# Performance work log

Measured on AMD Instinct MI355X. Metric: run time of the kernel, lower is better.

Reference implementation:

```python
import jax, jax.numpy as jnp
import numpy as np

B, H, L, D = 8, 16, 1024, 64

def setup_inputs() -> dict:
    key = jax.random.key(0)
    kq, kk, kv = jax.random.split(key, 3)
    q = jax.random.normal(kq, (B, H, L, D), dtype=jnp.float32)
    k = jax.random.normal(kk, (B, H, L, D), dtype=jnp.float32)
    v = jax.random.normal(kv, (B, H, L, D), dtype=jnp.float32)
    # causal mask, broadcast over batch and head
    mask = jnp.tril(jnp.ones((L, L), dtype=jnp.int32))[None, None, :, :]
    return {"q": q, "k": k, "v": v, "mask": mask}

def reference(q, k, v, mask):
    b, h, l, d = q.shape
    # FAITHFUL to original: k.view(b, h, d, l) is a reshape, NOT a transpose
    k_t = k.reshape(b, h, d, l)
    score = jnp.matmul(q, k_t) / np.sqrt(d).astype(np.float32)  # [b,h,l,l]
    # FAITHFUL to original bug: masked_fill(mask==0, -e) with e=1e-12
    score = jnp.where(mask == 0, jnp.float32(-1e-12), score)
    attn = jax.nn.softmax(score, axis=-1)
    out = jnp.matmul(attn, v)  # [b,h,l,d]
    return (out, attn)
```

## Files before the change

kernel.cpp:

```cpp
#include <hip/hip_runtime.h>

#define L_  1024
#define D_  64
#define TM  128
#define TN  64
#define LDK 72
#define NT  (L_ / TN)

typedef __attribute__((ext_vector_type(8))) short          short8;
typedef __attribute__((ext_vector_type(8))) unsigned short ushort8;
typedef __attribute__((ext_vector_type(4))) float          f32x4;

__device__ __forceinline__ unsigned short bf16r(float f) {
    unsigned u = __builtin_bit_cast(unsigned, f);
    u += 0x7fffu + ((u >> 16) & 1u);
    return (unsigned short)(u >> 16);
}

__device__ __forceinline__ void barrier_lds() {
    asm volatile("s_waitcnt lgkmcnt(0)" ::: "memory");
    __builtin_amdgcn_s_barrier();
}

__global__ __launch_bounds__(256, 2)
void sdpa_kernel(const float* __restrict__ q, const float* __restrict__ kmat,
                 const float* __restrict__ v, float* __restrict__ out,
                 float* __restrict__ attn)
{
    __shared__ __align__(16) unsigned short Qs[TM * LDK];
    __shared__ __align__(16) unsigned short Ks[2][TN * LDK];
    __shared__ __align__(16) unsigned short Vs[2][D_ * LDK];
    __shared__ __align__(16) unsigned short Ps[TM * LDK];

    const int t    = threadIdx.x;
    const int wave = t >> 6;
    const int lane = t & 63;
    const int quad = lane >> 4;
    const int l15  = lane & 15;
    const int bh   = blockIdx.x;
    const int rty  = blockIdx.y;

    const float* qb = q    + (size_t)bh * (L_ * D_);
    const float* kb = kmat + (size_t)bh * (L_ * D_);
    const float* vb = v    + (size_t)bh * (L_ * D_);
    float* outb  = out  + (size_t)bh * (L_ * D_);
    float* attnb = attn + (size_t)bh * ((size_t)L_ * L_);

    const int ng = t & 31, kg = t >> 5;
    float2 rK[8], rV[8];

    auto loadK = [&](int nt) {
        const float* src = kb + (size_t)(kg * 8) * L_ + nt * TN + 2 * ng;
        #pragma unroll
        for (int j = 0; j < 8; ++j) rK[j] = *(const float2*)(src + (size_t)j * L_);
    };
    auto writeK = [&](unsigned short* dst) {
        ushort8 r0, r1;
        #pragma unroll
        for (int j = 0; j < 8; ++j) { r0[j] = bf16r(rK[j].x); r1[j] = bf16r(rK[j].y); }
        *(ushort8*)&dst[(2 * ng)     * LDK + kg * 8] = r0;
        *(ushort8*)&dst[(2 * ng + 1) * LDK + kg * 8] = r1;
    };
    auto loadV = [&](int nt) {
        const float* src = vb + (size_t)(nt * TN + kg * 8) * D_ + 2 * ng;
        #pragma unroll
        for (int j = 0; j < 8; ++j) rV[j] = *(const float2*)(src + (size_t)j * D_);
    };
    auto writeV = [&](unsigned short* dst) {
        ushort8 r0, r1;
        #pragma unroll
        for (int j = 0; j < 8; ++j) { r0[j] = bf16r(rV[j].x); r1[j] = bf16r(rV[j].y); }
        *(ushort8*)&dst[(2 * ng)     * LDK + kg * 8] = r0;
        *(ushort8*)&dst[(2 * ng + 1) * LDK + kg * 8] = r1;
    };

    const int rowA = wave * 32;

    auto computeScoreT = [&](f32x4 (&acc)[2][4], const unsigned short* ksrc) {
        #pragma unroll
        for (int ks = 0; ks < 2; ++ks) {
            const int cu = ks * 32 + quad * 8;
            short8 af[2];
            #pragma unroll
            for (int tr = 0; tr < 2; ++tr)
                af[tr] = *(const short8*)&Qs[(rowA + tr * 16 + l15) * LDK + cu];
            #pragma unroll
            for (int tc = 0; tc < 4; ++tc) {
                short8 bfr = *(const short8*)&ksrc[(tc * 16 + l15) * LDK + cu];
                #pragma unroll
                for (int tr = 0; tr < 2; ++tr)
                    acc[tr][tc] = __builtin_amdgcn_mfma_f32_16x16x32_bf16(bfr, af[tr], acc[tr][tc], 0, 0, 0);
            }
        }
    };

    const f32x4 zero4 = {0.f, 0.f, 0.f, 0.f};

    for (int pass = 0; pass < 2; ++pass) {
        const int rt = (pass == 0) ? rty : (7 - rty);
        const int m0 = rt * TM;

        barrier_lds();

        #pragma unroll
        for (int i = 0; i < 8; ++i) {
            int idx = (i * 256 + t) * 4;
            int m = idx >> 6, c = idx & 63;
            float4 f = *(const float4*)&qb[(size_t)(m0 + m) * D_ + c];
            ushort4 b;
            b.x = bf16r(f.x); b.y = bf16r(f.y); b.z = bf16r(f.z); b.w = bf16r(f.w);
            *(ushort4*)&Qs[m * LDK + c] = b;
        }

        float zpart[2][4] = {};
        const int ntmax1 = (m0 + TM - 1) / TN;
        loadK(0); writeK(Ks[0]);
        for (int nt = 0; nt <= ntmax1; ++nt) {
            barrier_lds();
            if (nt < ntmax1) loadK(nt + 1);
            f32x4 acc[2][4];
            #pragma unroll
            for (int tr = 0; tr < 2; ++tr)
                #pragma unroll
                for (int tc = 0; tc < 4; ++tc) acc[tr][tc] = zero4;
            computeScoreT(acc, Ks[nt & 1]);
            #pragma unroll
            for (int tr = 0; tr < 2; ++tr) {
                const int gm = m0 + rowA + tr * 16 + l15;
                #pragma unroll
                for (int tc = 0; tc < 4; ++tc)
                    #pragma unroll
                    for (int r = 0; r < 4; ++r) {
                        const int gn = nt * TN + tc * 16 + quad * 4 + r;
                        zpart[tr][tc] += (gn > gm) ? 1.0f : __expf(acc[tr][tc][r] * 0.125f);
                    }
            }
            if (nt < ntmax1) writeK(Ks[(nt + 1) & 1]);
        }
        const float zmissing = (float)(L_ - (ntmax1 + 1) * TN);

        loadK(0); loadV(0);
        float rcpz[2];
        #pragma unroll
        for (int tr = 0; tr < 2; ++tr) {
            float z = (zpart[tr][0] + zpart[tr][1]) + (zpart[tr][2] + zpart[tr][3]);
            z += __shfl_xor(z, 16);
            z += __shfl_xor(z, 32);
            rcpz[tr] = 1.0f / (z + zmissing);
        }
        barrier_lds();
        writeK(Ks[0]); writeV(Vs[0]);

        f32x4 oacc[2][4];
        #pragma unroll
        for (int tr = 0; tr < 2; ++tr)
            #pragma unroll
            for (int tc = 0; tc < 4; ++tc) oacc[tr][tc] = zero4;

        for (int nt = 0; nt < NT; ++nt) {
            const bool fullmask = (nt * TN) > (m0 + TM - 1);
            barrier_lds();
            const int nn = nt + 1;
            const bool nextV = (nn < NT);
            const bool nextK = nextV && ((nn * TN) <= (m0 + TM - 1));
            if (nextV) loadV(nn);
            if (nextK) loadK(nn);

            if (!fullmask) {
                f32x4 acc[2][4];
                #pragma unroll
                for (int tr = 0; tr < 2; ++tr)
                    #pragma unroll
                    for (int tc = 0; tc < 4; ++tc) acc[tr][tc] = zero4;
                computeScoreT(acc, Ks[nt & 1]);
                #pragma unroll
                for (int tr = 0; tr < 2; ++tr) {
                    const int lrow = rowA + tr * 16 + l15;
                    const int gm = m0 + lrow;
                    const float rz = rcpz[tr];
                    #pragma unroll
                    for (int tc = 0; tc < 4; ++tc) {
                        float p[4];
                        #pragma unroll
                        for (int r = 0; r < 4; ++r) {
                            const int gn = nt * TN + tc * 16 + quad * 4 + r;
                            float e = (gn > gm) ? 1.0f : __expf(acc[tr][tc][r] * 0.125f);
                            p[r] = e * rz;
                        }
                        float4 vv = {p[0], p[1], p[2], p[3]};
                        *(float4*)&attnb[(size_t)gm * L_ + nt * TN + tc * 16 + quad * 4] = vv;
                        ushort4 pw;
                        pw.x = bf16r(p[0]); pw.y = bf16r(p[1]);
                        pw.z = bf16r(p[2]); pw.w = bf16r(p[3]);
                        *(ushort4*)&Ps[lrow * LDK + tc * 16 + quad * 4] = pw;
                    }
                }
            } else {
                const bool firstFull = (nt == ntmax1 + 1);
                #pragma unroll
                for (int tr = 0; tr < 2; ++tr) {
                    const int lrow = rowA + tr * 16 + l15;
                    const int gm = m0 + lrow;
                    const float rz = rcpz[tr];
                    float4 vv = {rz, rz, rz, rz};
                    const unsigned short pb = bf16r(rz);
                    ushort4 p4; p4.x = pb; p4.y = pb; p4.z = pb; p4.w = pb;
                    #pragma unroll
                    for (int c = 0; c < 4; ++c) {
                        *(float4*)&attnb[(size_t)gm * L_ + nt * TN + c * 16 + quad * 4] = vv;
                        if (firstFull)
                            *(ushort4*)&Ps[lrow * LDK + c * 16 + quad * 4] = p4;
                    }
                }
            }

            #pragma unroll
            for (int ks = 0; ks < 2; ++ks) {
                const int cu = ks * 32 + quad * 8;
                short8 pf[2];
                #pragma unroll
                for (int tr = 0; tr < 2; ++tr)
                    pf[tr] = *(const short8*)&Ps[(rowA + tr * 16 + l15) * LDK + cu];
                #pragma unroll
                for (int tc = 0; tc < 4; ++tc) {
                    short8 vf = *(const short8*)&Vs[nt & 1][(tc * 16 + l15) * LDK + cu];
                    #pragma unroll
                    for (int tr = 0; tr < 2; ++tr)
                        oacc[tr][tc] = __builtin_amdgcn_mfma_f32_16x16x32_bf16(pf[tr], vf, oacc[tr][tc], 0, 0, 0);
                }
            }

            if (nextV) writeV(Vs[nn & 1]);
            if (nextK) writeK(Ks[nn & 1]);
        }

        #pragma unroll
        for (int tr = 0; tr < 2; ++tr)
            #pragma unroll
            for (int r = 0; r < 4; ++r) {
                const int gm = m0 + rowA + tr * 16 + quad * 4 + r;
                #pragma unroll
                for (int tc = 0; tc < 4; ++tc)
                    outb[(size_t)gm * D_ + tc * 16 + l15] = oacc[tr][tc][r];
            }
    }
}

extern "C" void kernel_launch(void* const* d_in, const int* in_sizes, int n_in,
                              void* d_out, int out_size, void* d_ws, size_t ws_size,
                              hipStream_t stream) {
    (void)in_sizes; (void)n_in; (void)d_ws; (void)ws_size; (void)out_size;
    const float* q = (const float*)d_in[0];
    const float* k = (const float*)d_in[1];
    const float* v = (const float*)d_in[2];
    float* out  = (float*)d_out;
    float* attn = (float*)d_out + (size_t)8 * 16 * 1024 * 64;
    dim3 grid(128, 4);
    sdpa_kernel<<<grid, dim3(256), 0, stream>>>(q, k, v, out, attn);
}
```

Measured before the change: 698.3 us.

## Fuse both row-tile passes into one loop sharing K/V tiles, keep Q in registers

Each block handles two query row tiles (rty and 7-rty). It now processes both in a single sweep over K/V tiles instead of two sequential passes, so every staged K/V tile is loaded, converted and barrier-synchronised once and used for both row tiles. The Q fragments move out of LDS into registers, preloaded once per block, which frees the Qs buffer and removes the per-pass Q staging. In exchange register pressure roughly doubles for the output accumulators and Q fragments under the 2-blocks-per-CU launch bound, which risks spills. Ps is also rewritten on every fully masked tile, because it is now shared between the two row tiles.

```diff
diff --git a/kernel.cpp b/kernel.cpp
--- a/kernel.cpp
+++ b/kernel.cpp
@@ -27,7 +27,6 @@
                  const float* __restrict__ v, float* __restrict__ out,
                  float* __restrict__ attn)
 {
-    __shared__ __align__(16) unsigned short Qs[TM * LDK];
     __shared__ __align__(16) unsigned short Ks[2][TN * LDK];
     __shared__ __align__(16) unsigned short Vs[2][D_ * LDK];
     __shared__ __align__(16) unsigned short Ps[TM * LDK];
@@ -39,6 +38,10 @@
     const int l15  = lane & 15;
     const int bh   = blockIdx.x;
     const int rty  = blockIdx.y;
+    const int m0A  = rty * TM;
+    const int m0B  = (7 - rty) * TM;
+    const int ntmaxA = 2 * rty + 1;
+    const int ntmaxB = 15 - 2 * rty;
 
     const float* qb = q    + (size_t)bh * (L_ * D_);
     const float* kb = kmat + (size_t)bh * (L_ * D_);
@@ -46,6 +49,30 @@
     float* outb  = out  + (size_t)bh * (L_ * D_);
     float* attnb = attn + (size_t)bh * ((size_t)L_ * L_);
 
+    const int rowA = wave * 32;
+
+    short8 qA[2][2], qB[2][2];
+    {
+        auto ldq = [&](int m0, short8 (&qr)[2][2]) {
+            #pragma unroll
+            for (int tr = 0; tr < 2; ++tr)
+                #pragma unroll
+                for (int ks = 0; ks < 2; ++ks) {
+                    const float* src = qb + (size_t)(m0 + rowA + tr * 16 + l15) * D_ + ks * 32 + quad * 8;
+                    float4 a = *(const float4*)src;
+                    float4 b = *(const float4*)(src + 4);
+                    short8 r;
+                    r[0] = (short)bf16r(a.x); r[1] = (short)bf16r(a.y);
+                    r[2] = (short)bf16r(a.z); r[3] = (short)bf16r(a.w);
+                    r[4] = (short)bf16r(b.x); r[5] = (short)bf16r(b.y);
+                    r[6] = (short)bf16r(b.z); r[7] = (short)bf16r(b.w);
+                    qr[tr][ks] = r;
+                }
+        };
+        ldq(m0A, qA);
+        ldq(m0B, qB);
+    }
+
     const int ng = t & 31, kg = t >> 5;
     float2 rK[8], rV[8];
 
@@ -74,176 +101,177 @@
         *(ushort8*)&dst[(2 * ng + 1) * LDK + kg * 8] = r1;
     };
 
-    const int rowA = wave * 32;
-
-    auto computeScoreT = [&](f32x4 (&acc)[2][4], const unsigned short* ksrc) {
+    auto computeScoreT = [&](f32x4 (&acc)[2][4], const short8 (&qr)[2][2],
+                             const unsigned short* ksrc) {
         #pragma unroll
         for (int ks = 0; ks < 2; ++ks) {
             const int cu = ks * 32 + quad * 8;
-            short8 af[2];
-            #pragma unroll
-            for (int tr = 0; tr < 2; ++tr)
-                af[tr] = *(const short8*)&Qs[(rowA + tr * 16 + l15) * LDK + cu];
             #pragma unroll
             for (int tc = 0; tc < 4; ++tc) {
                 short8 bfr = *(const short8*)&ksrc[(tc * 16 + l15) * LDK + cu];
                 #pragma unroll
                 for (int tr = 0; tr < 2; ++tr)
-                    acc[tr][tc] = __builtin_amdgcn_mfma_f32_16x16x32_bf16(bfr, af[tr], acc[tr][tc], 0, 0, 0);
+                    acc[tr][tc] = __builtin_amdgcn_mfma_f32_16x16x32_bf16(bfr, qr[tr][ks], acc[tr][tc], 0, 0, 0);
             }
         }
     };
 
     const f32x4 zero4 = {0.f, 0.f, 0.f, 0.f};
 
-    for (int pass = 0; pass < 2; ++pass) {
-        const int rt = (pass == 0) ? rty : (7 - rty);
-        const int m0 = rt * TM;
-
+    float zpA[2][4] = {}, zpB[2][4] = {};
+    auto accumZ = [&](f32x4 (&acc)[2][4], float (&zp)[2][4], int m0, int nt) {
+        #pragma unroll
+        for (int tr = 0; tr < 2; ++tr) {
+            const int gm = m0 + rowA + tr * 16 + l15;
+            #pragma unroll
+            for (int tc = 0; tc < 4; ++tc)
+                #pragma unroll
+                for (int r = 0; r < 4; ++r) {
+                    const int gn = nt * TN + tc * 16 + quad * 4 + r;
+                    zp[tr][tc] += (gn > gm) ? 1.0f : __expf(acc[tr][tc][r] * 0.125f);
+                }
+        }
+    };
+
+    loadK(0); writeK(Ks[0]);
+    for (int nt = 0; nt <= ntmaxB; ++nt) {
         barrier_lds();
-
-        #pragma unroll
-        for (int i = 0; i < 8; ++i) {
-            int idx = (i * 256 + t) * 4;
-            int m = idx >> 6, c = idx & 63;
-            float4 f = *(const float4*)&qb[(size_t)(m0 + m) * D_ + c];
-            ushort4 b;
-            b.x = bf16r(f.x); b.y = bf16r(f.y); b.z = bf16r(f.z); b.w = bf16r(f.w);
-            *(ushort4*)&Qs[m * LDK + c] = b;
-        }
-
-        float zpart[2][4] = {};
-        const int ntmax1 = (m0 + TM - 1) / TN;
-        loadK(0); writeK(Ks[0]);
-        for (int nt = 0; nt <= ntmax1; ++nt) {
-            barrier_lds();
-            if (nt < ntmax1) loadK(nt + 1);
+        if (nt < ntmaxB) loadK(nt + 1);
+        if (nt <= ntmaxA) {
             f32x4 acc[2][4];
             #pragma unroll
             for (int tr = 0; tr < 2; ++tr)
                 #pragma unroll
                 for (int tc = 0; tc < 4; ++tc) acc[tr][tc] = zero4;
-            computeScoreT(acc, Ks[nt & 1]);
+            computeScoreT(acc, qA, Ks[nt & 1]);
+            accumZ(acc, zpA, m0A, nt);
+        }
+        {
+            f32x4 acc[2][4];
+            #pragma unroll
+            for (int tr = 0; tr < 2; ++tr)
+                #pragma unroll
+                for (int tc = 0; tc < 4; ++tc) acc[tr][tc] = zero4;
+            computeScoreT(acc, qB, Ks[nt & 1]);
+            accumZ(acc, zpB, m0B, nt);
+        }
+        if (nt < ntmaxB) writeK(Ks[(nt + 1) & 1]);
+    }
+    const float zmissA = (float)(L_ - (ntmaxA + 1) * TN);
+    const float zmissB = (float)(L_ - (ntmaxB + 1) * TN);
+
+    loadK(0); loadV(0);
+    float rcpzA[2], rcpzB[2];
+    #pragma unroll
+    for (int tr = 0; tr < 2; ++tr) {
+        float za = (zpA[tr][0] + zpA[tr][1]) + (zpA[tr][2] + zpA[tr][3]);
+        za += __shfl_xor(za, 16);
+        za += __shfl_xor(za, 32);
+        rcpzA[tr] = 1.0f / (za + zmissA);
+        float zb = (zpB[tr][0] + zpB[tr][1]) + (zpB[tr][2] + zpB[tr][3]);
+        zb += __shfl_xor(zb, 16);
+        zb += __shfl_xor(zb, 32);
+        rcpzB[tr] = 1.0f / (zb + zmissB);
+    }
+    barrier_lds();
+    writeK(Ks[0]); writeV(Vs[0]);
+
+    f32x4 oA[2][4], oB[2][4];
+    #pragma unroll
+    for (int tr = 0; tr < 2; ++tr)
+        #pragma unroll
+        for (int tc = 0; tc < 4; ++tc) { oA[tr][tc] = zero4; oB[tr][tc] = zero4; }
+
+    auto doTile = [&](int nt, int m0, int ntmaxv, const short8 (&qr)[2][2],
+                      const float (&rz)[2], f32x4 (&oacc)[2][4]) {
+        if (nt <= ntmaxv) {
+            f32x4 acc[2][4];
+            #pragma unroll
+            for (int tr = 0; tr < 2; ++tr)
+                #pragma unroll
+                for (int tc = 0; tc < 4; ++tc) acc[tr][tc] = zero4;
+            computeScoreT(acc, qr, Ks[nt & 1]);
             #pragma unroll
             for (int tr = 0; tr < 2; ++tr) {
-                const int gm = m0 + rowA + tr * 16 + l15;
-                #pragma unroll
-                for (int tc = 0; tc < 4; ++tc)
+                const int lrow = rowA + tr * 16 + l15;
+                const int gm = m0 + lrow;
+                const float rzv = rz[tr];
+                #pragma unroll
+                for (int tc = 0; tc < 4; ++tc) {
+                    float p[4];
                     #pragma unroll
                     for (int r = 0; r < 4; ++r) {
                         const int gn = nt * TN + tc * 16 + quad * 4 + r;
-                        zpart[tr][tc] += (gn > gm) ? 1.0f : __expf(acc[tr][tc][r] * 0.125f);
+                        float e = (gn > gm) ? 1.0f : __expf(acc[tr][tc][r] * 0.125f);
+                        p[r] = e * rzv;
                     }
-            }
-            if (nt < ntmax1) writeK(Ks[(nt + 1) & 1]);
-        }
-        const float zmissing = (float)(L_ - (ntmax1 + 1) * TN);
-
-        loadK(0); loadV(0);
-        float rcpz[2];
-        #pragma unroll
-        for (int tr = 0; tr < 2; ++tr) {
-            float z = (zpart[tr][0] + zpart[tr][1]) + (zpart[tr][2] + zpart[tr][3]);
-            z += __shfl_xor(z, 16);
-            z += __shfl_xor(z, 32);
-            rcpz[tr] = 1.0f / (z + zmissing);
-        }
+                    float4 vv = {p[0], p[1], p[2], p[3]};
+                    *(float4*)&attnb[(size_t)gm * L_ + nt * TN + tc * 16 + quad * 4] = vv;
+                    ushort4 pw;
+                    pw.x = bf16r(p[0]); pw.y = bf16r(p[1]);
+                    pw.z = bf16r(p[2]); pw.w = bf16r(p[3]);
+                    *(ushort4*)&Ps[lrow * LDK + tc * 16 + quad * 4] = pw;
+                }
+            }
+        } else {
+            #pragma unroll
+            for (int tr = 0; tr < 2; ++tr) {
+                const int lrow = rowA + tr * 16 + l15;
+                const int gm = m0 + lrow;
+                const float rzv = rz[tr];
+                float4 vv = {rzv, rzv, rzv, rzv};
+                const unsigned short pb = bf16r(rzv);
+                ushort4 p4; p4.x = pb; p4.y = pb; p4.z = pb; p4.w = pb;
+                #pragma unroll
+                for (int c = 0; c < 4; ++c) {
+                    *(float4*)&attnb[(size_t)gm * L_ + nt * TN + c * 16 + quad * 4] = vv;
+                    *(ushort4*)&Ps[lrow * LDK + c * 16 + quad * 4] = p4;
+                }
+            }
+        }
+        #pragma unroll
+        for (int ks = 0; ks < 2; ++ks) {
+            const int cu = ks * 32 + quad * 8;
+            short8 pf[2];
+            #pragma unroll
+            for (int tr = 0; tr < 2; ++tr)
+                pf[tr] = *(const short8*)&Ps[(rowA + tr * 16 + l15) * LDK + cu];
+            #pragma unroll
+            for (int tc = 0; tc < 4; ++tc) {
+                short8 vf = *(const short8*)&Vs[nt & 1][(tc * 16 + l15) * LDK + cu];
+                #pragma unroll
+                for (int tr = 0; tr < 2; ++tr)
+                    oacc[tr][tc] = __builtin_amdgcn_mfma_f32_16x16x32_bf16(pf[tr], vf, oacc[tr][tc], 0, 0, 0);
+            }
+        }
+    };
+
+    for (int nt = 0; nt < NT; ++nt) {
         barrier_lds();
-        writeK(Ks[0]); writeV(Vs[0]);
-
-        f32x4 oacc[2][4];
-        #pragma unroll
-        for (int tr = 0; tr < 2; ++tr)
-            #pragma unroll
-            for (int tc = 0; tc < 4; ++tc) oacc[tr][tc] = zero4;
-
-        for (int nt = 0; nt < NT; ++nt) {
-            const bool fullmask = (nt * TN) > (m0 + TM - 1);
-            barrier_lds();
-            const int nn = nt + 1;
-            const bool nextV = (nn < NT);
-            const bool nextK = nextV && ((nn * TN) <= (m0 + TM - 1));
-            if (nextV) loadV(nn);
-            if (nextK) loadK(nn);
-
-            if (!fullmask) {
-                f32x4 acc[2][4];
-                #pragma unroll
-                for (int tr = 0; tr < 2; ++tr)
-                    #pragma unroll
-                    for (int tc = 0; tc < 4; ++tc) acc[tr][tc] = zero4;
-                computeScoreT(acc, Ks[nt & 1]);
-                #pragma unroll
-                for (int tr = 0; tr < 2; ++tr) {
-                    const int lrow = rowA + tr * 16 + l15;
-                    const int gm = m0 + lrow;
-                    const float rz = rcpz[tr];
-                    #pragma unroll
-                    for (int tc = 0; tc < 4; ++tc) {
-                        float p[4];
-                        #pragma unroll
-                        for (int r = 0; r < 4; ++r) {
-                            const int gn = nt * TN + tc * 16 + quad * 4 + r;
-                            float e = (gn > gm) ? 1.0f : __expf(acc[tr][tc][r] * 0.125f);
-                            p[r] = e * rz;
-                        }
-                        float4 vv = {p[0], p[1], p[2], p[3]};
-                        *(float4*)&attnb[(size_t)gm * L_ + nt * TN + tc * 16 + quad * 4] = vv;
-                        ushort4 pw;
-                        pw.x = bf16r(p[0]); pw.y = bf16r(p[1]);
-                        pw.z = bf16r(p[2]); pw.w = bf16r(p[3]);
-                        *(ushort4*)&Ps[lrow * LDK + tc * 16 + quad * 4] = pw;
-                    }
-                }
-            } else {
-                const bool firstFull = (nt == ntmax1 + 1);
-                #pragma unroll
-                for (int tr = 0; tr < 2; ++tr) {
-                    const int lrow = rowA + tr * 16 + l15;
-                    const int gm = m0 + lrow;
-                    const float rz = rcpz[tr];
-                    float4 vv = {rz, rz, rz, rz};
-                    const unsigned short pb = bf16r(rz);
-                    ushort4 p4; p4.x = pb; p4.y = pb; p4.z = pb; p4.w = pb;
-                    #pragma unroll
-                    for (int c = 0; c < 4; ++c) {
-                        *(float4*)&attnb[(size_t)gm * L_ + nt * TN + c * 16 + quad * 4] = vv;
-                        if (firstFull)
-                            *(ushort4*)&Ps[lrow * LDK + c * 16 + quad * 4] = p4;
-                    }
-                }
-            }
-
-            #pragma unroll
-            for (int ks = 0; ks < 2; ++ks) {
-                const int cu = ks * 32 + quad * 8;
-                short8 pf[2];
-                #pragma unroll
-                for (int tr = 0; tr < 2; ++tr)
-                    pf[tr] = *(const short8*)&Ps[(rowA + tr * 16 + l15) * LDK + cu];
-                #pragma unroll
-                for (int tc = 0; tc < 4; ++tc) {
-                    short8 vf = *(const short8*)&Vs[nt & 1][(tc * 16 + l15) * LDK + cu];
-                    #pragma unroll
-                    for (int tr = 0; tr < 2; ++tr)
-                        oacc[tr][tc] = __builtin_amdgcn_mfma_f32_16x16x32_bf16(pf[tr], vf, oacc[tr][tc], 0, 0, 0);
-                }
-            }
-
-            if (nextV) writeV(Vs[nn & 1]);
-            if (nextK) writeK(Ks[nn & 1]);
-        }
-
-        #pragma unroll
-        for (int tr = 0; tr < 2; ++tr)
-            #pragma unroll
-            for (int r = 0; r < 4; ++r) {
-                const int gm = m0 + rowA + tr * 16 + quad * 4 + r;
-                #pragma unroll
-                for (int tc = 0; tc < 4; ++tc)
-                    outb[(size_t)gm * D_ + tc * 16 + l15] = oacc[tr][tc][r];
-            }
-    }
+        const int nn = nt + 1;
+        const bool nextV = (nn < NT);
+        const bool nextK = nextV && (nn <= ntmaxB);
+        if (nextV) loadV(nn);
+        if (nextK) loadK(nn);
+
+        doTile(nt, m0A, ntmaxA, qA, rcpzA, oA);
+        doTile(nt, m0B, ntmaxB, qB, rcpzB, oB);
+
+        if (nextV) writeV(Vs[nn & 1]);
+        if (nextK) writeK(Ks[nn & 1]);
+    }
+
+    #pragma unroll
+    for (int tr = 0; tr < 2; ++tr)
+        #pragma unroll
+        for (int r = 0; r < 4; ++r) {
+            const int lr = rowA + tr * 16 + quad * 4 + r;
+            #pragma unroll
+            for (int tc = 0; tc < 4; ++tc) {
+                outb[(size_t)(m0A + lr) * D_ + tc * 16 + l15] = oA[tr][tc][r];
+                outb[(size_t)(m0B + lr) * D_ + tc * 16 + l15] = oB[tr][tc][r];
+            }
+        }
 }
 
 extern "C" void kernel_launch(void* const* d_in, const int* in_sizes, int n_in,
```

After: 742.8 us. +6.4%, slower.

## Use 8 waves per block with 16 rows each instead of 4 waves with 32

Applied to the files above, without the earlier changes.

Doubles the block to 512 threads so each wave handles one 16-row MFMA strip instead of two, halving per-thread accumulators and K/V staging registers. Global-to-LDS loads are spread over more threads. The aim is more waves in flight to hide memory latency on the attn write and K/V loads, at the cost of each wave reusing its K/V fragments across fewer rows and more LDS reads per MFMA.

```diff
diff --git a/kernel.cpp b/kernel.cpp
--- a/kernel.cpp
+++ b/kernel.cpp
@@ -8,7 +8,7 @@
 #define NT  (L_ / TN)
 
 typedef __attribute__((ext_vector_type(8))) short          short8;
-typedef __attribute__((ext_vector_type(8))) unsigned short ushort8;
+typedef __attribute__((ext_vector_type(4))) unsigned short ushort4e;
 typedef __attribute__((ext_vector_type(4))) float          f32x4;
 
 __device__ __forceinline__ unsigned short bf16r(float f) {
@@ -22,7 +22,7 @@
     __builtin_amdgcn_s_barrier();
 }
 
-__global__ __launch_bounds__(256, 2)
+__global__ __launch_bounds__(512, 4)
 void sdpa_kernel(const float* __restrict__ q, const float* __restrict__ kmat,
                  const float* __restrict__ v, float* __restrict__ out,
                  float* __restrict__ attn)
@@ -37,6 +37,7 @@
     const int lane = t & 63;
     const int quad = lane >> 4;
     const int l15  = lane & 15;
+    const int wrow = wave * 16;
     const int bh   = blockIdx.x;
     const int rty  = blockIdx.y;
 
@@ -47,49 +48,42 @@
     float* attnb = attn + (size_t)bh * ((size_t)L_ * L_);
 
     const int ng = t & 31, kg = t >> 5;
-    float2 rK[8], rV[8];
+    float2 rK[4], rV[4];
 
     auto loadK = [&](int nt) {
-        const float* src = kb + (size_t)(kg * 8) * L_ + nt * TN + 2 * ng;
-        #pragma unroll
-        for (int j = 0; j < 8; ++j) rK[j] = *(const float2*)(src + (size_t)j * L_);
+        const float* src = kb + (size_t)(kg * 4) * L_ + nt * TN + 2 * ng;
+        #pragma unroll
+        for (int j = 0; j < 4; ++j) rK[j] = *(const float2*)(src + (size_t)j * L_);
     };
     auto writeK = [&](unsigned short* dst) {
-        ushort8 r0, r1;
-        #pragma unroll
-        for (int j = 0; j < 8; ++j) { r0[j] = bf16r(rK[j].x); r1[j] = bf16r(rK[j].y); }
-        *(ushort8*)&dst[(2 * ng)     * LDK + kg * 8] = r0;
-        *(ushort8*)&dst[(2 * ng + 1) * LDK + kg * 8] = r1;
+        ushort4e r0, r1;
+        #pragma unroll
+        for (int j = 0; j < 4; ++j) { r0[j] = bf16r(rK[j].x); r1[j] = bf16r(rK[j].y); }
+        *(ushort4e*)&dst[(2 * ng)     * LDK + kg * 4] = r0;
+        *(ushort4e*)&dst[(2 * ng + 1) * LDK + kg * 4] = r1;
     };
     auto loadV = [&](int nt) {
-        const float* src = vb + (size_t)(nt * TN + kg * 8) * D_ + 2 * ng;
-        #pragma unroll
-        for (int j = 0; j < 8; ++j) rV[j] = *(const float2*)(src + (size_t)j * D_);
+        const float* src = vb + (size_t)(nt * TN + kg * 4) * D_ + 2 * ng;
+        #pragma unroll
+        for (int j = 0; j < 4; ++j) rV[j] = *(const float2*)(src + (size_t)j * D_);
     };
     auto writeV = [&](unsigned short* dst) {
-        ushort8 r0, r1;
-        #pragma unroll
-        for (int j = 0; j < 8; ++j) { r0[j] = bf16r(rV[j].x); r1[j] = bf16r(rV[j].y); }
-        *(ushort8*)&dst[(2 * ng)     * LDK + kg * 8] = r0;
-        *(ushort8*)&dst[(2 * ng + 1) * LDK + kg * 8] = r1;
-    };
-
-    const int rowA = wave * 32;
-
-    auto computeScoreT = [&](f32x4 (&acc)[2][4], const unsigned short* ksrc) {
+        ushort4e r0, r1;
+        #pragma unroll
+        for (int j = 0; j < 4; ++j) { r0[j] = bf16r(rV[j].x); r1[j] = bf16r(rV[j].y); }
+        *(ushort4e*)&dst[(2 * ng)     * LDK + kg * 4] = r0;
+        *(ushort4e*)&dst[(2 * ng + 1) * LDK + kg * 4] = r1;
+    };
+
+    auto computeScoreT = [&](f32x4 (&acc)[4], const unsigned short* ksrc) {
         #pragma unroll
         for (int ks = 0; ks < 2; ++ks) {
             const int cu = ks * 32 + quad * 8;
-            short8 af[2];
-            #pragma unroll
-            for (int tr = 0; tr < 2; ++tr)
-                af[tr] = *(const short8*)&Qs[(rowA + tr * 16 + l15) * LDK + cu];
+            short8 af = *(const short8*)&Qs[(wrow + l15) * LDK + cu];
             #pragma unroll
             for (int tc = 0; tc < 4; ++tc) {
                 short8 bfr = *(const short8*)&ksrc[(tc * 16 + l15) * LDK + cu];
-                #pragma unroll
-                for (int tr = 0; tr < 2; ++tr)
-                    acc[tr][tc] = __builtin_amdgcn_mfma_f32_16x16x32_bf16(bfr, af[tr], acc[tr][tc], 0, 0, 0);
+                acc[tc] = __builtin_amdgcn_mfma_f32_16x16x32_bf16(bfr, af, acc[tc], 0, 0, 0);
             }
         }
     };
@@ -103,59 +97,51 @@
         barrier_lds();
 
         #pragma unroll
-        for (int i = 0; i < 8; ++i) {
-            int idx = (i * 256 + t) * 4;
+        for (int i = 0; i < 4; ++i) {
+            int idx = (i * 512 + t) * 4;
             int m = idx >> 6, c = idx & 63;
             float4 f = *(const float4*)&qb[(size_t)(m0 + m) * D_ + c];
-            ushort4 b;
-            b.x = bf16r(f.x); b.y = bf16r(f.y); b.z = bf16r(f.z); b.w = bf16r(f.w);
-            *(ushort4*)&Qs[m * LDK + c] = b;
-        }
-
-        float zpart[2][4] = {};
+            ushort4e b;
+            b[0] = bf16r(f.x); b[1] = bf16r(f.y); b[2] = bf16r(f.z); b[3] = bf16r(f.w);
+            *(ushort4e*)&Qs[m * LDK + c] = b;
+        }
+
+        float zpart[4] = {};
         const int ntmax1 = (m0 + TM - 1) / TN;
         loadK(0); writeK(Ks[0]);
         for (int nt = 0; nt <= ntmax1; ++nt) {
             barrier_lds();
             if (nt < ntmax1) loadK(nt + 1);
-            f32x4 acc[2][4];
-            #pragma unroll
-            for (int tr = 0; tr < 2; ++tr)
-                #pragma unroll
-                for (int tc = 0; tc < 4; ++tc) acc[tr][tc] = zero4;
+            f32x4 acc[4];
+            #pragma unroll
+            for (int tc = 0; tc < 4; ++tc) acc[tc] = zero4;
             computeScoreT(acc, Ks[nt & 1]);
-            #pragma unroll
-            for (int tr = 0; tr < 2; ++tr) {
-                const int gm = m0 + rowA + tr * 16 + l15;
-                #pragma unroll
-                for (int tc = 0; tc < 4; ++tc)
-                    #pragma unroll
-                    for (int r = 0; r < 4; ++r) {
-                        const int gn = nt * TN + tc * 16 + quad * 4 + r;
-                        zpart[tr][tc] += (gn > gm) ? 1.0f : __expf(acc[tr][tc][r] * 0.125f);
-                    }
-            }
+            const int gm = m0 + wrow + l15;
+            #pragma unroll
+            for (int tc = 0; tc < 4; ++tc)
+                #pragma unroll
+                for (int r = 0; r < 4; ++r) {
+                    const int gn = nt * TN + tc * 16 + quad * 4 + r;
+                    zpart[tc] += (gn > gm) ? 1.0f : __expf(acc[tc][r] * 0.125f);
+                }
             if (nt < ntmax1) writeK(Ks[(nt + 1) & 1]);
         }
         const float zmissing = (float)(L_ - (ntmax1 + 1) * TN);
 
         loadK(0); loadV(0);
-        float rcpz[2];
-        #pragma unroll
-        for (int tr = 0; tr < 2; ++tr) {
-            float z = (zpart[tr][0] + zpart[tr][1]) + (zpart[tr][2] + zpart[tr][3]);
+        float rcpz;
+        {
+            float z = (zpart[0] + zpart[1]) + (zpart[2] + zpart[3]);
             z += __shfl_xor(z, 16);
             z += __shfl_xor(z, 32);
-            rcpz[tr] = 1.0f / (z + zmissing);
+            rcpz = 1.0f / (z + zmissing);
         }
         barrier_lds();
         writeK(Ks[0]); writeV(Vs[0]);
 
-        f32x4 oacc[2][4];
-        #pragma unroll
-        for (int tr = 0; tr < 2; ++tr)
-            #pragma unroll
-            for (int tc = 0; tc < 4; ++tc) oacc[tr][tc] = zero4;
+        f32x4 oacc[4];
+        #pragma unroll
+        for (int tc = 0; tc < 4; ++tc) oacc[tc] = zero4;
 
         for (int nt = 0; nt < NT; ++nt) {
             const bool fullmask = (nt * TN) > (m0 + TM - 1);
@@ -167,66 +153,51 @@
             if (nextK) loadK(nn);
 
             if (!fullmask) {
-                f32x4 acc[2][4];
-                #pragma unroll
-                for (int tr = 0; tr < 2; ++tr)
+                f32x4 acc[4];
+                #pragma unroll
+                for (int tc = 0; tc < 4; ++tc) acc[tc] = zero4;
+                computeScoreT(acc, Ks[nt & 1]);
+                const int lrow = wrow + l15;
+                const int gm = m0 + lrow;
+                #pragma unroll
+                for (int tc = 0; tc < 4; ++tc) {
+                    float p[4];
                     #pragma unroll
-                    for (int tc = 0; tc < 4; ++tc) acc[tr][tc] = zero4;
-                computeScoreT(acc, Ks[nt & 1]);
-                #pragma unroll
-                for (int tr = 0; tr < 2; ++tr) {
-                    const int lrow = rowA + tr * 16 + l15;
-                    const int gm = m0 + lrow;
-                    const float rz = rcpz[tr];
-                    #pragma unroll
-                    for (int tc = 0; tc < 4; ++tc) {
-                        float p[4];
-                        #pragma unroll
-                        for (int r = 0; r < 4; ++r) {
-                            const int gn = nt * TN + tc * 16 + quad * 4 + r;
-                            float e = (gn > gm) ? 1.0f : __expf(acc[tr][tc][r] * 0.125f);
-                            p[r] = e * rz;
-                        }
-                        float4 vv = {p[0], p[1], p[2], p[3]};
-                        *(float4*)&attnb[(size_t)gm * L_ + nt * TN + tc * 16 + quad * 4] = vv;
-                        ushort4 pw;
-                        pw.x = bf16r(p[0]); pw.y = bf16r(p[1]);
-                        pw.z = bf16r(p[2]); pw.w = bf16r(p[3]);
-                        *(ushort4*)&Ps[lrow * LDK + tc * 16 + quad * 4] = pw;
+                    for (int r = 0; r < 4; ++r) {
+                        const int gn = nt * TN + tc * 16 + quad * 4 + r;
+                        float e = (gn > gm) ? 1.0f : __expf(acc[tc][r] * 0.125f);
+                        p[r] = e * rcpz;
                     }
+                    float4 vv = {p[0], p[1], p[2], p[3]};
+                    *(float4*)&attnb[(size_t)gm * L_ + nt * TN + tc * 16 + quad * 4] = vv;
+                    ushort4e pw;
+                    pw[0] = bf16r(p[0]); pw[1] = bf16r(p[1]);
+                    pw[2] = bf16r(p[2]); pw[3] = bf16r(p[3]);
+                    *(ushort4e*)&Ps[lrow * LDK + tc * 16 + quad * 4] = pw;
                 }
             } else {
                 const bool firstFull = (nt == ntmax1 + 1);
-                #pragma unroll
-                for (int tr = 0; tr < 2; ++tr) {
-                    const int lrow = rowA + tr * 16 + l15;
-                    const int gm = m0 + lrow;
-                    const float rz = rcpz[tr];
-                    float4 vv = {rz, rz, rz, rz};
-                    const unsigned short pb = bf16r(rz);
-                    ushort4 p4; p4.x = pb; p4.y = pb; p4.z = pb; p4.w = pb;
-                    #pragma unroll
-                    for (int c = 0; c < 4; ++c) {
-                        *(float4*)&attnb[(size_t)gm * L_ + nt * TN + c * 16 + quad * 4] = vv;
-                        if (firstFull)
-                            *(ushort4*)&Ps[lrow * LDK + c * 16 + quad * 4] = p4;
-                    }
+                const int lrow = wrow + l15;
+                const int gm = m0 + lrow;
+                float4 vv = {rcpz, rcpz, rcpz, rcpz};
+                const unsigned short pb = bf16r(rcpz);
+                ushort4e p4; p4[0] = pb; p4[1] = pb; p4[2] = pb; p4[3] = pb;
+                #pragma unroll
+                for (int c = 0; c < 4; ++c) {
+                    *(float4*)&attnb[(size_t)gm * L_ + nt * TN + c * 16 + quad * 4] = vv;
+                    if (firstFull)
+                        *(ushort4e*)&Ps[lrow * LDK + c * 16 + quad * 4] = p4;
                 }
             }
 
             #pragma unroll
             for (int ks = 0; ks < 2; ++ks) {
                 const int cu = ks * 32 + quad * 8;
-                short8 pf[2];
-                #pragma unroll
-                for (int tr = 0; tr < 2; ++tr)
-                    pf[tr] = *(const short8*)&Ps[(rowA + tr * 16 + l15) * LDK + cu];
+                short8 pf = *(const short8*)&Ps[(wrow + l15) * LDK + cu];
                 #pragma unroll
                 for (int tc = 0; tc < 4; ++tc) {
                     short8 vf = *(const short8*)&Vs[nt & 1][(tc * 16 + l15) * LDK + cu];
-                    #pragma unroll
-                    for (int tr = 0; tr < 2; ++tr)
-                        oacc[tr][tc] = __builtin_amdgcn_mfma_f32_16x16x32_bf16(pf[tr], vf, oacc[tr][tc], 0, 0, 0);
+                    oacc[tc] = __builtin_amdgcn_mfma_f32_16x16x32_bf16(pf, vf, oacc[tc], 0, 0, 0);
                 }
             }
 
@@ -235,14 +206,12 @@
         }
 
         #pragma unroll
-        for (int tr = 0; tr < 2; ++tr)
-            #pragma unroll
-            for (int r = 0; r < 4; ++r) {
-                const int gm = m0 + rowA + tr * 16 + quad * 4 + r;
-                #pragma unroll
-                for (int tc = 0; tc < 4; ++tc)
-                    outb[(size_t)gm * D_ + tc * 16 + l15] = oacc[tr][tc][r];
-            }
+        for (int r = 0; r < 4; ++r) {
+            const int gm = m0 + wrow + quad * 4 + r;
+            #pragma unroll
+            for (int tc = 0; tc < 4; ++tc)
+                outb[(size_t)gm * D_ + tc * 16 + l15] = oacc[tc][r];
+        }
     }
 }
 
@@ -256,5 +225,5 @@
     float* out  = (float*)d_out;
     float* attn = (float*)d_out + (size_t)8 * 16 * 1024 * 64;
     dim3 grid(128, 4);
-    sdpa_kernel<<<grid, dim3(256), 0, stream>>>(q, k, v, out, attn);
-}
+    sdpa_kernel<<<grid, dim3(512), 0, stream>>>(q, k, v, out, attn);
+}
```

After: 714.1 us. 2.3% more time.

## Split softmax normalizer computation into a separate pre-pass kernel

Applied to the files above, without the earlier changes.

Moves the first pass, which computes each row's softmax denominator, into its own kernel. That kernel launches one block per 128-row tile (1024 blocks) at higher occupancy and stores the reciprocal in the first column of the output buffer. The main kernel then reads that value back instead of recomputing the QK^T sum, which shortens its critical path and spreads the first-pass work across more blocks. The cost is an extra launch and a global round trip through the output buffer as scratch. The scheme relies on the main kernel overwriting that column later and reading it before any write.

```diff
diff --git a/kernel.cpp b/kernel.cpp
--- a/kernel.cpp
+++ b/kernel.cpp
@@ -20,6 +20,108 @@
 __device__ __forceinline__ void barrier_lds() {
     asm volatile("s_waitcnt lgkmcnt(0)" ::: "memory");
     __builtin_amdgcn_s_barrier();
+}
+
+__global__ __launch_bounds__(256, 4)
+void z_kernel(const float* __restrict__ q, const float* __restrict__ kmat,
+              float* __restrict__ out)
+{
+    __shared__ __align__(16) unsigned short Qs[TM * LDK];
+    __shared__ __align__(16) unsigned short Ks[2][TN * LDK];
+
+    const int t    = threadIdx.x;
+    const int wave = t >> 6;
+    const int lane = t & 63;
+    const int quad = lane >> 4;
+    const int l15  = lane & 15;
+    const int bh   = blockIdx.x;
+    const int rt   = blockIdx.y;
+    const int m0   = rt * TM;
+    const int rowA = wave * 32;
+
+    const float* qb = q    + (size_t)bh * (L_ * D_);
+    const float* kb = kmat + (size_t)bh * (L_ * D_);
+    float* outb = out + (size_t)bh * (L_ * D_);
+
+    #pragma unroll
+    for (int i = 0; i < 8; ++i) {
+        int idx = (i * 256 + t) * 4;
+        int m = idx >> 6, c = idx & 63;
+        float4 f = *(const float4*)&qb[(size_t)(m0 + m) * D_ + c];
+        ushort4 b;
+        b.x = bf16r(f.x); b.y = bf16r(f.y); b.z = bf16r(f.z); b.w = bf16r(f.w);
+        *(ushort4*)&Qs[m * LDK + c] = b;
+    }
+
+    const int ng = t & 31, kg = t >> 5;
+    float2 rK[8];
+    auto loadK = [&](int nt) {
+        const float* src = kb + (size_t)(kg * 8) * L_ + nt * TN + 2 * ng;
+        #pragma unroll
+        for (int j = 0; j < 8; ++j) rK[j] = *(const float2*)(src + (size_t)j * L_);
+    };
+    auto writeK = [&](unsigned short* dst) {
+        ushort8 r0, r1;
+        #pragma unroll
+        for (int j = 0; j < 8; ++j) { r0[j] = bf16r(rK[j].x); r1[j] = bf16r(rK[j].y); }
+        *(ushort8*)&dst[(2 * ng)     * LDK + kg * 8] = r0;
+        *(ushort8*)&dst[(2 * ng + 1) * LDK + kg * 8] = r1;
+    };
+
+    auto computeScoreT = [&](f32x4 (&acc)[2][4], const unsigned short* ksrc) {
+        #pragma unroll
+        for (int ks = 0; ks < 2; ++ks) {
+            const int cu = ks * 32 + quad * 8;
+            short8 af[2];
+            #pragma unroll
+            for (int tr = 0; tr < 2; ++tr)
+                af[tr] = *(const short8*)&Qs[(rowA + tr * 16 + l15) * LDK + cu];
+            #pragma unroll
+            for (int tc = 0; tc < 4; ++tc) {
+                short8 bfr = *(const short8*)&ksrc[(tc * 16 + l15) * LDK + cu];
+                #pragma unroll
+                for (int tr = 0; tr < 2; ++tr)
+                    acc[tr][tc] = __builtin_amdgcn_mfma_f32_16x16x32_bf16(bfr, af[tr], acc[tr][tc], 0, 0, 0);
+            }
+        }
+    };
+
+    const f32x4 zero4 = {0.f, 0.f, 0.f, 0.f};
+    float zpart[2][4] = {};
+    const int ntmax1 = (m0 + TM - 1) / TN;
+    loadK(0); writeK(Ks[0]);
+    for (int nt = 0; nt <= ntmax1; ++nt) {
+        barrier_lds();
+        if (nt < ntmax1) loadK(nt + 1);
+        f32x4 acc[2][4];
+        #pragma unroll
+        for (int tr = 0; tr < 2; ++tr)
+            #pragma unroll
+            for (int tc = 0; tc < 4; ++tc) acc[tr][tc] = zero4;
+        computeScoreT(acc, Ks[nt & 1]);
+        #pragma unroll
+        for (int tr = 0; tr < 2; ++tr) {
+            const int gm = m0 + rowA + tr * 16 + l15;
+            #pragma unroll
+            for (int tc = 0; tc < 4; ++tc)
+                #pragma unroll
+                for (int r = 0; r < 4; ++r) {
+                    const int gn = nt * TN + tc * 16 + quad * 4 + r;
+                    zpart[tr][tc] += (gn > gm) ? 1.0f : __expf(acc[tr][tc][r] * 0.125f);
+                }
+        }
+        if (nt < ntmax1) writeK(Ks[(nt + 1) & 1]);
+    }
+    const float zmissing = (float)(L_ - (ntmax1 + 1) * TN);
+    #pragma unroll
+    for (int tr = 0; tr < 2; ++tr) {
+        float z = (zpart[tr][0] + zpart[tr][1]) + (zpart[tr][2] + zpart[tr][3]);
+        z += __shfl_xor(z, 16);
+        z += __shfl_xor(z, 32);
+        const float rcpz = 1.0f / (z + zmissing);
+        if (quad == 0)
+            outb[(size_t)(m0 + rowA + tr * 16 + l15) * D_] = rcpz;
+    }
 }
 
 __global__ __launch_bounds__(256, 2)
@@ -39,6 +141,7 @@
     const int l15  = lane & 15;
     const int bh   = blockIdx.x;
     const int rty  = blockIdx.y;
+    const int rowA = wave * 32;
 
     const float* qb = q    + (size_t)bh * (L_ * D_);
     const float* kb = kmat + (size_t)bh * (L_ * D_);
@@ -48,7 +151,6 @@
 
     const int ng = t & 31, kg = t >> 5;
     float2 rK[8], rV[8];
-
     auto loadK = [&](int nt) {
         const float* src = kb + (size_t)(kg * 8) * L_ + nt * TN + 2 * ng;
         #pragma unroll
@@ -74,8 +176,6 @@
         *(ushort8*)&dst[(2 * ng + 1) * LDK + kg * 8] = r1;
     };
 
-    const int rowA = wave * 32;
-
     auto computeScoreT = [&](f32x4 (&acc)[2][4], const unsigned short* ksrc) {
         #pragma unroll
         for (int ks = 0; ks < 2; ++ks) {
@@ -99,6 +199,7 @@
     for (int pass = 0; pass < 2; ++pass) {
         const int rt = (pass == 0) ? rty : (7 - rty);
         const int m0 = rt * TM;
+        const int ntmax1 = (m0 + TM - 1) / TN;
 
         barrier_lds();
 
@@ -111,43 +212,12 @@
             b.x = bf16r(f.x); b.y = bf16r(f.y); b.z = bf16r(f.z); b.w = bf16r(f.w);
             *(ushort4*)&Qs[m * LDK + c] = b;
         }
-
-        float zpart[2][4] = {};
-        const int ntmax1 = (m0 + TM - 1) / TN;
-        loadK(0); writeK(Ks[0]);
-        for (int nt = 0; nt <= ntmax1; ++nt) {
-            barrier_lds();
-            if (nt < ntmax1) loadK(nt + 1);
-            f32x4 acc[2][4];
-            #pragma unroll
-            for (int tr = 0; tr < 2; ++tr)
-                #pragma unroll
-                for (int tc = 0; tc < 4; ++tc) acc[tr][tc] = zero4;
-            computeScoreT(acc, Ks[nt & 1]);
-            #pragma unroll
-            for (int tr = 0; tr < 2; ++tr) {
-                const int gm = m0 + rowA + tr * 16 + l15;
-                #pragma unroll
-                for (int tc = 0; tc < 4; ++tc)
-                    #pragma unroll
-                    for (int r = 0; r < 4; ++r) {
-                        const int gn = nt * TN + tc * 16 + quad * 4 + r;
-                        zpart[tr][tc] += (gn > gm) ? 1.0f : __expf(acc[tr][tc][r] * 0.125f);
-                    }
-            }
-            if (nt < ntmax1) writeK(Ks[(nt + 1) & 1]);
-        }
-        const float zmissing = (float)(L_ - (ntmax1 + 1) * TN);
-
         loadK(0); loadV(0);
         float rcpz[2];
         #pragma unroll
-        for (int tr = 0; tr < 2; ++tr) {
-            float z = (zpart[tr][0] + zpart[tr][1]) + (zpart[tr][2] + zpart[tr][3]);
-            z += __shfl_xor(z, 16);
-            z += __shfl_xor(z, 32);
-            rcpz[tr] = 1.0f / (z + zmissing);
-        }
+        for (int tr = 0; tr < 2; ++tr)
+            rcpz[tr] = outb[(size_t)(m0 + rowA + tr * 16 + l15) * D_];
+
         barrier_lds();
         writeK(Ks[0]); writeV(Vs[0]);
 
@@ -255,6 +325,6 @@
     const float* v = (const float*)d_in[2];
     float* out  = (float*)d_out;
     float* attn = (float*)d_out + (size_t)8 * 16 * 1024 * 64;
-    dim3 grid(128, 4);
-    sdpa_kernel<<<grid, dim3(256), 0, stream>>>(q, k, v, out, attn);
-}
+    z_kernel<<<dim3(128, 8), dim3(256), 0, stream>>>(q, k, out);
+    sdpa_kernel<<<dim3(128, 4), dim3(256), 0, stream>>>(q, k, v, out, attn);
+}
```

Result: slower. 755.3 us (+8.2%).
